# Performance work log

Measured on AMD Instinct MI355X. Metric: run time of the kernel, lower is better.

The kernel has to match this reference:

```python
import jax, jax.numpy as jnp
import numpy as np

B, T, E, H = 4, 2048, 1024, 16
D = E // H
PAD_TOKEN_ID = 0
VOCAB = 50257


def setup_inputs() -> dict:
    key = jax.random.key(0)
    k1, k2, k3, k4 = jax.random.split(key, 4)
    x = jax.random.normal(k1, (B, T, E), dtype=jnp.float32)
    input_ids = jax.random.randint(k2, (B, T), 0, VOCAB, dtype=jnp.int64)
    # guarantee first key of every sequence is non-pad so no softmax row is fully masked
    input_ids = input_ids.at[:, 0].set(1)
    w_qkv = jax.random.normal(k3, (E, 3 * E), dtype=jnp.float32) * 0.02
    w_out = jax.random.normal(k4, (E, E), dtype=jnp.float32) * 0.02
    b_out = jnp.zeros((E,), dtype=jnp.float32)
    return {"x": x, "input_ids": input_ids, "w_qkv": w_qkv, "w_out": w_out, "b_out": b_out}


def reference(x, input_ids, w_qkv, w_out, b_out):
    b, t, e = x.shape
    # fused QKV projection (bias=False in original)
    qkv = x @ w_qkv                                   # [B,T,3E]
    q, k, v = jnp.split(qkv, 3, axis=-1)
    q = q.reshape(b, t, H, D).transpose(0, 2, 1, 3)   # [B,H,T,D]
    k = k.reshape(b, t, H, D).transpose(0, 2, 1, 3)
    v = v.reshape(b, t, H, D).transpose(0, 2, 1, 3)

    scale = 1.0 / jnp.sqrt(jnp.asarray(D, dtype=x.dtype))
    scores = jnp.einsum("bhqd,bhkd->bhqk", q, k) * scale   # [B,H,T,T]

    causal = jnp.tril(jnp.ones((t, t), dtype=bool))         # [T,T]
    key_keep = (input_ids != PAD_TOKEN_ID)[:, None, None, :]  # [B,1,1,T]
    mask = causal[None, None, :, :] & key_keep               # [B,1(T broadcast over H),T,T]
    scores = jnp.where(mask, scores, -jnp.inf)

    attn = jax.nn.softmax(scores, axis=-1)                   # dropout_p=0 in eval
    y = jnp.einsum("bhqk,bhkd->bhqd", attn, v)               # [B,H,T,D]
    y = y.transpose(0, 2, 1, 3).reshape(b, t, e)             # [B,T,E]
    return y @ w_out + b_out
```

## Files before the change

kernel.cpp:

```cpp
#include <hip/hip_runtime.h>
#include <hip/hip_bf16.h>
#include <stdint.h>

#define Hn 16
#define Tn 2048
#define En 1024
#define Dh 64

typedef __bf16 bf16x8 __attribute__((ext_vector_type(8)));
typedef float f32x4 __attribute__((ext_vector_type(4)));
typedef unsigned short u16;
typedef u16 u16x8 __attribute__((ext_vector_type(8)));

#define SCALE_Q 0.18033688f

__device__ __forceinline__ u16 f2bf(float f) {
  __bf16 b = (__bf16)f;
  return __builtin_bit_cast(u16, b);
}

typedef const __attribute__((address_space(1))) void gvoid_t;
typedef __attribute__((address_space(3))) void lvoid_t;
__device__ __forceinline__ void gl_lds16(const void* g, void* l) {
  __builtin_amdgcn_global_load_lds((gvoid_t*)g, (lvoid_t*)l, 16, 0, 0);
}

__global__ void prep_k(const float* __restrict__ x, u16* __restrict__ xb,
                       const int* __restrict__ ids, u16* __restrict__ maskh,
                       const float* __restrict__ wqkv, u16* __restrict__ wqkvt,
                       const float* __restrict__ wout, u16* __restrict__ woutt) {
  __shared__ float tile[32][33];
  __shared__ int is64_s;
  const int blk = blockIdx.x;
  const int tid = threadIdx.x;

  if (blk < 4096) {
    int i = (blk * 256 + tid) * 8;
    float4 a = *(const float4*)(x + i);
    float4 b = *(const float4*)(x + i + 4);
    u16x8 o;
    o[0] = f2bf(a.x); o[1] = f2bf(a.y); o[2] = f2bf(a.z); o[3] = f2bf(a.w);
    o[4] = f2bf(b.x); o[5] = f2bf(b.y); o[6] = f2bf(b.z); o[7] = f2bf(b.w);
    *(u16x8*)(xb + i) = o;
    return;
  }
  if (blk < 4128) {
    if (tid == 0) {
      int all0 = 1;
      for (int i = 1; i < 256; i += 2) all0 &= (ids[i] == 0);
      is64_s = all0;
    }
    __syncthreads();
    int i = (blk - 4096) * 256 + tid;
    int v = is64_s ? ids[2 * i] : ids[i];
    maskh[i] = (v != 0) ? (u16)0 : f2bf(-1e30f);
    return;
  }
  const int t = blk - 4128;
  const int bx = t & 127, by = t >> 7;
  const float* in; u16* out; int C, c0;
  if (bx < 96) { in = wqkv; out = wqkvt; C = 3072; c0 = bx * 32; }
  else         { in = wout; out = woutt; C = 1024; c0 = (bx - 96) * 32; }
  const int r0 = by * 32;
  const int tx = tid & 31, ty = tid >> 5;
  for (int i = ty; i < 32; i += 8)
    tile[i][tx] = in[(size_t)(r0 + i) * C + c0 + tx];
  __syncthreads();
  for (int i = ty; i < 32; i += 8)
    out[(size_t)(c0 + i) * 1024 + r0 + tx] = f2bf(tile[tx][i]);
}

__device__ __forceinline__ void gemm_mainloop(const u16* __restrict__ A,
                                              const u16* __restrict__ Bt,
                                              int K, int m0, int n0,
                                              u16* lds, f32x4 acc[4][4]) {
  const int tid = threadIdx.x;
  const int lane = tid & 63;
  const int w = tid >> 6;
  const int wm = (w >> 1) * 64, wn = (w & 1) * 64;
  const int quad = lane >> 4, ln = lane & 15;

  const int e0 = w * 512 + lane * 8;
  const int r0 = e0 >> 5;
  const int cS = (e0 & 31) ^ (((r0 >> 1) & 3) * 8);

  const u16* gA = A + (size_t)(m0 + r0) * K + cS;
  const u16* gB = Bt + (size_t)(n0 + r0) * K + cS;
  const int xR = ((ln >> 1) & 3) * 8;

  auto stage = [&](int buf, int k0) {
    u16* lA = lds + buf * 8192 + e0;
    u16* lB = lA + 4096;
    gl_lds16(gA + k0, lA);
    gl_lds16(gA + (size_t)64 * K + k0, lA + 2048);
    gl_lds16(gB + k0, lB);
    gl_lds16(gB + (size_t)64 * K + k0, lB + 2048);
  };

  stage(0, 0);
  int cur = 0;
  for (int k0 = 0; k0 < K; k0 += 32) {
    __syncthreads();
    if (k0 + 32 < K) stage(cur ^ 1, k0 + 32);
    const u16* lb = lds + cur * 8192;
    bf16x8 af[4], bfr[4];
#pragma unroll
    for (int mt = 0; mt < 4; mt++)
      af[mt] = *(const bf16x8*)(lb + (wm + mt * 16 + ln) * 32 + ((quad * 8) ^ xR));
#pragma unroll
    for (int nt = 0; nt < 4; nt++)
      bfr[nt] = *(const bf16x8*)(lb + 4096 + (wn + nt * 16 + ln) * 32 + ((quad * 8) ^ xR));
#pragma unroll
    for (int mt = 0; mt < 4; mt++)
#pragma unroll
      for (int nt = 0; nt < 4; nt++)
        acc[mt][nt] = __builtin_amdgcn_mfma_f32_16x16x32_bf16(af[mt], bfr[nt],
                                                              acc[mt][nt], 0, 0, 0);
    cur ^= 1;
  }
  __syncthreads();
}

__global__ __launch_bounds__(256, 4)
void gemm_qkv_kernel(const u16* __restrict__ X, const u16* __restrict__ Wt,
                     u16* __restrict__ Qo, u16* __restrict__ Ko,
                     u16* __restrict__ Vto) {
  __shared__ __align__(16) u16 lds[128 * 130];
  const int m0 = blockIdx.y * 128, n0 = blockIdx.x * 128;
  f32x4 acc[4][4];
#pragma unroll
  for (int i = 0; i < 4; i++)
#pragma unroll
    for (int j = 0; j < 4; j++) acc[i][j] = (f32x4){0.f, 0.f, 0.f, 0.f};

  gemm_mainloop(X, Wt, En, m0, n0, lds, acc);

  const int tid = threadIdx.x, lane = tid & 63, w = tid >> 6;
  const int wm = (w >> 1) * 64, wn = (w & 1) * 64;
  const int quad = lane >> 4, ln = lane & 15;
  const int which = n0 >> 10;
  const int bb = m0 >> 11, t0 = m0 & (Tn - 1);

  if (which < 2) {
#pragma unroll
    for (int mt = 0; mt < 4; mt++)
#pragma unroll
      for (int nt = 0; nt < 4; nt++)
#pragma unroll
        for (int r = 0; r < 4; r++) {
          int t = t0 + wm + mt * 16 + quad * 4 + r;
          int ng = n0 + wn + nt * 16 + ln;
          int e = ng & (En - 1);
          int h = e >> 6, d = e & 63;
          size_t bh = (size_t)(bb * Hn + h);
          if (which == 0)
            Qo[(bh * Tn + t) * Dh + d] = f2bf(acc[mt][nt][r] * SCALE_Q);
          else
            Ko[(bh * Tn + t) * Dh + d] = f2bf(acc[mt][nt][r]);
        }
  } else {
#pragma unroll
    for (int mt = 0; mt < 4; mt++)
#pragma unroll
      for (int nt = 0; nt < 4; nt++)
#pragma unroll
        for (int r = 0; r < 4; r++)
          lds[(wm + mt * 16 + quad * 4 + r) * 130 + wn + nt * 16 + ln] =
              f2bf(acc[mt][nt][r]);
    __syncthreads();
    const int ebase = n0 & (En - 1);
#pragma unroll
    for (int i = 0; i < 32; i++) {
      int col = w * 32 + i;
      int e = ebase + col;
      int hh = e >> 6, d = e & 63;
      size_t vrow = (((size_t)(bb * Hn + hh)) * Dh + d) * Tn + t0;
      Vto[vrow + lane] = lds[lane * 130 + col];
      Vto[vrow + 64 + lane] = lds[(64 + lane) * 130 + col];
    }
  }
}

__global__ __launch_bounds__(256, 4)
void gemm_out_kernel(const u16* __restrict__ Y, const u16* __restrict__ Wt,
                     const float* __restrict__ bias, float* __restrict__ Out) {
  __shared__ __align__(16) u16 lds[16384];
  const int m0 = blockIdx.y * 128, n0 = blockIdx.x * 128;
  f32x4 acc[4][4];
#pragma unroll
  for (int i = 0; i < 4; i++)
#pragma unroll
    for (int j = 0; j < 4; j++) acc[i][j] = (f32x4){0.f, 0.f, 0.f, 0.f};

  gemm_mainloop(Y, Wt, En, m0, n0, lds, acc);

  const int tid = threadIdx.x, lane = tid & 63, w = tid >> 6;
  const int wm = (w >> 1) * 64, wn = (w & 1) * 64;
  const int quad = lane >> 4, ln = lane & 15;

#pragma unroll
  for (int mt = 0; mt < 4; mt++)
#pragma unroll
    for (int nt = 0; nt < 4; nt++)
#pragma unroll
      for (int r = 0; r < 4; r++) {
        int mg = m0 + wm + mt * 16 + quad * 4 + r;
        int ng = n0 + wn + nt * 16 + ln;
        Out[(size_t)mg * En + ng] = acc[mt][nt][r] + bias[ng];
      }
}

__global__ __launch_bounds__(256, 3)
void attn_kernel(const u16* __restrict__ Q, const u16* __restrict__ K,
                 const u16* __restrict__ Vt, const u16* __restrict__ maskh,
                 u16* __restrict__ Y) {
  __shared__ __align__(16) u16 Pl[128 * 76];
  __shared__ __align__(16) u16 KL[2 * 4096];
  __shared__ __align__(16) u16 ML[2048];

  const int bid = blockIdx.x;
  const int g = bid >> 8, sq = (bid >> 6) & 3;
  int qt;
  if (g == 0)      qt = 15 - sq;
  else if (g == 1) qt = sq;
  else if (g == 2) qt = 11 - sq;
  else             qt = 4 + sq;
  const int bh = bid & 63;
  const int b = bh >> 4, h = bh & 15;
  const int tid = threadIdx.x, lane = tid & 63, w = tid >> 6;
  const int quad = lane >> 4, ln = lane & 15;
  const int qb = w * 32;
  const int g0 = qt * 128 + qb;

  const size_t baseQK = (size_t)bh * (Tn * Dh);
  const size_t baseV = (size_t)bh * (Dh * Tn);
  const u16* Kp = K + baseQK;

  const int srow = tid >> 3;
  const int scol = ((tid & 7) * 8) ^ ((srow & 7) * 8);
  const u16* gK0 = Kp + (size_t)srow * Dh + scol;
  const u16* gK1 = Kp + (size_t)(srow + 32) * Dh + scol;
  u16* lK0 = KL + tid * 8;
  u16* lK1 = lK0 + 2048;

  auto stage = [&](int buf, int k0) {
    gl_lds16(gK0 + (size_t)k0 * Dh, lK0 + buf * 4096);
    gl_lds16(gK1 + (size_t)k0 * Dh, lK1 + buf * 4096);
  };

  gl_lds16(maskh + (size_t)b * Tn + tid * 8, ML + tid * 8);

  bf16x8 aq[2][2];
#pragma unroll
  for (int rt = 0; rt < 2; rt++)
#pragma unroll
    for (int ks = 0; ks < 2; ks++)
      aq[rt][ks] = *(const bf16x8*)(Q + baseQK +
          (size_t)(g0 + rt * 16 + ln) * Dh + ks * 32 + quad * 8);

  bf16x8 onesb;
#pragma unroll
  for (int i = 0; i < 8; i++) onesb[i] = (__bf16)1.0f;

  f32x4 O[2][4];
  f32x4 ls[2];
#pragma unroll
  for (int rt = 0; rt < 2; rt++) {
#pragma unroll
    for (int dt = 0; dt < 4; dt++) O[rt][dt] = (f32x4){0.f, 0.f, 0.f, 0.f};
    ls[rt] = (f32x4){0.f, 0.f, 0.f, 0.f};
  }

  auto tile = [&](const u16* kl, int k0, bool dg) {
    f32x4 s[2][4];
    {
      bf16x8 bk[4][2];
      float kvf[4];
#pragma unroll
      for (int ct = 0; ct < 4; ct++) {
        kvf[ct] = __builtin_bit_cast(float,
                      (uint32_t)ML[k0 + ct * 16 + ln] << 16);
#pragma unroll
        for (int ks = 0; ks < 2; ks++)
          bk[ct][ks] = *(const bf16x8*)(kl + (ct * 16 + ln) * 64 +
                                        ((ks * 32 + quad * 8) ^ ((ln & 7) * 8)));
      }
#pragma unroll
      for (int rt = 0; rt < 2; rt++)
#pragma unroll
        for (int ct = 0; ct < 4; ct++)
          s[rt][ct] = (f32x4){kvf[ct], kvf[ct], kvf[ct], kvf[ct]};
      __builtin_amdgcn_s_setprio(1);
#pragma unroll
      for (int ks = 0; ks < 2; ks++)
#pragma unroll
        for (int rt = 0; rt < 2; rt++)
#pragma unroll
          for (int ct = 0; ct < 4; ct++)
            s[rt][ct] = __builtin_amdgcn_mfma_f32_16x16x32_bf16(aq[rt][ks], bk[ct][ks],
                                                                s[rt][ct], 0, 0, 0);
      __builtin_amdgcn_s_setprio(0);
    }

    bf16x8 bv[4][2];
#pragma unroll
    for (int dt = 0; dt < 4; dt++)
#pragma unroll
      for (int ks = 0; ks < 2; ks++)
        bv[dt][ks] = *(const bf16x8*)(Vt + baseV +
            (size_t)(dt * 16 + ln) * Tn + k0 + ks * 32 + quad * 8);

#pragma unroll
    for (int rt = 0; rt < 2; rt++) {
      if (dg) {
#pragma unroll
        for (int ct = 0; ct < 4; ct++)
#pragma unroll
          for (int r = 0; r < 4; r++) {
            int qg = g0 + rt * 16 + quad * 4 + r;
            int kg = k0 + ct * 16 + ln;
            float v = (kg > qg) ? -1e30f : s[rt][ct][r];
            float p = exp2f(v);
            Pl[(qb + rt * 16 + quad * 4 + r) * 76 + ct * 16 + ln] = f2bf(p);
          }
      } else {
#pragma unroll
        for (int ct = 0; ct < 4; ct++)
#pragma unroll
          for (int r = 0; r < 4; r++) {
            float p = exp2f(s[rt][ct][r]);
            Pl[(qb + rt * 16 + quad * 4 + r) * 76 + ct * 16 + ln] = f2bf(p);
          }
      }
    }

    __builtin_amdgcn_s_setprio(1);
#pragma unroll
    for (int ks2 = 0; ks2 < 2; ks2++)
#pragma unroll
      for (int rt = 0; rt < 2; rt++) {
        bf16x8 ap = *(const bf16x8*)(Pl + (qb + rt * 16 + ln) * 76 + ks2 * 32 + quad * 8);
#pragma unroll
        for (int dt = 0; dt < 4; dt++)
          O[rt][dt] = __builtin_amdgcn_mfma_f32_16x16x32_bf16(ap, bv[dt][ks2],
                                                              O[rt][dt], 0, 0, 0);
        ls[rt] = __builtin_amdgcn_mfma_f32_16x16x32_bf16(ap, onesb,
                                                         ls[rt], 0, 0, 0);
      }
    __builtin_amdgcn_s_setprio(0);
  };

  const int nfull = g0 >> 6;
  const int NT = 2 * qt + 1;
  stage(0, 0);
  int cur = 0;
  for (int kt = 0; kt <= NT; kt++) {
    __syncthreads();
    if (kt < NT) stage(cur ^ 1, (kt + 1) * 64);
    if (kt < nfull)       tile(KL + cur * 4096, kt * 64, false);
    else if (kt == nfull) tile(KL + cur * 4096, kt * 64, true);
    cur ^= 1;
  }

#pragma unroll
  for (int rt = 0; rt < 2; rt++)
#pragma unroll
    for (int r = 0; r < 4; r++) {
      float inv = 1.f / ls[rt][r];
      int tg = g0 + rt * 16 + quad * 4 + r;
      size_t ob = ((size_t)b * Tn + tg) * En + h * Dh;
#pragma unroll
      for (int dt = 0; dt < 4; dt++)
        Y[ob + dt * 16 + ln] = f2bf(O[rt][dt][r] * inv);
    }
}

#define OFF_MASK  0
#define OFF_WQKVT 16384
#define OFF_WOUTT (OFF_WQKVT + 3145728)
#define OFF_Q     (OFF_WOUTT + 1048576)
#define OFF_K     (OFF_Q + 8388608)
#define OFF_XY    (OFF_K + 8388608)

extern "C" void kernel_launch(void* const* d_in, const int* in_sizes, int n_in,
                              void* d_out, int out_size, void* d_ws, size_t ws_size,
                              hipStream_t stream) {
  const float* x = nullptr;
  const int* ids_raw = nullptr;
  const float* wqkv = nullptr;
  const float* wout = nullptr;
  const float* bias = nullptr;
  for (int i = 0; i < n_in; i++) {
    switch (in_sizes[i]) {
      case 8388608: x = (const float*)d_in[i]; break;
      case 8192:    ids_raw = (const int*)d_in[i]; break;
      case 3145728: wqkv = (const float*)d_in[i]; break;
      case 1048576: wout = (const float*)d_in[i]; break;
      case 1024:    bias = (const float*)d_in[i]; break;
      default: break;
    }
  }
  if (!x) x = (const float*)d_in[0];
  if (!ids_raw) ids_raw = (const int*)d_in[1];
  if (!wqkv) wqkv = (const float*)d_in[2];
  if (!wout) wout = (const float*)d_in[3];
  if (!bias) bias = (const float*)d_in[4];

  u16* ws = (u16*)d_ws;
  u16* maskh = ws + OFF_MASK;
  u16* wqkv_t = ws + OFF_WQKVT;
  u16* wout_t = ws + OFF_WOUTT;
  u16* Qb = ws + OFF_Q;
  u16* Kb = ws + OFF_K;
  u16* XbYb = ws + OFF_XY;
  u16* Vtb = (u16*)d_out;
  float* out = (float*)d_out;

  prep_k<<<8224, 256, 0, stream>>>(x, XbYb, ids_raw, maskh,
                                   wqkv, wqkv_t, wout, wout_t);
  gemm_qkv_kernel<<<dim3(24, 64), 256, 0, stream>>>(XbYb, wqkv_t, Qb, Kb, Vtb);
  attn_kernel<<<1024, 256, 0, stream>>>(Qb, Kb, Vtb, maskh, XbYb);
  gemm_out_kernel<<<dim3(8, 64), 256, 0, stream>>>(XbYb, wout_t, bias, out);
}
```

Before: 264.1 us.

## Halve attention query tile to 64 rows and launch 2048 blocks longest-first

Each attention block now handles a 64-row query tile, one 16-row slice per wave, instead of 128 rows with two slices per wave. The grid doubles to 2048 blocks, scheduled in descending causal length. The paired triangle scheduling is replaced by a simple longest-first order. This aims at finer load balance and lower register and LDS use for higher occupancy, at the cost of each K/V tile being reused by fewer query rows, so K and V are loaded twice as often per query.

```diff
diff --git a/kernel.cpp b/kernel.cpp
--- a/kernel.cpp
+++ b/kernel.cpp
@@ -214,23 +214,18 @@
 void attn_kernel(const u16* __restrict__ Q, const u16* __restrict__ K,
                  const u16* __restrict__ Vt, const u16* __restrict__ maskh,
                  u16* __restrict__ Y) {
-  __shared__ __align__(16) u16 Pl[128 * 76];
+  __shared__ __align__(16) u16 Pl[64 * 76];
   __shared__ __align__(16) u16 KL[2 * 4096];
   __shared__ __align__(16) u16 ML[2048];
 
   const int bid = blockIdx.x;
-  const int g = bid >> 8, sq = (bid >> 6) & 3;
-  int qt;
-  if (g == 0)      qt = 15 - sq;
-  else if (g == 1) qt = sq;
-  else if (g == 2) qt = 11 - sq;
-  else             qt = 4 + sq;
+  const int qt2 = 31 - (bid >> 6);
   const int bh = bid & 63;
   const int b = bh >> 4, h = bh & 15;
   const int tid = threadIdx.x, lane = tid & 63, w = tid >> 6;
   const int quad = lane >> 4, ln = lane & 15;
-  const int qb = w * 32;
-  const int g0 = qt * 128 + qb;
+  const int qb = w * 16;
+  const int g0 = qt2 * 64 + qb;
 
   const size_t baseQK = (size_t)bh * (Tn * Dh);
   const size_t baseV = (size_t)bh * (Dh * Tn);
@@ -250,29 +245,23 @@
 
   gl_lds16(maskh + (size_t)b * Tn + tid * 8, ML + tid * 8);
 
-  bf16x8 aq[2][2];
-#pragma unroll
-  for (int rt = 0; rt < 2; rt++)
-#pragma unroll
-    for (int ks = 0; ks < 2; ks++)
-      aq[rt][ks] = *(const bf16x8*)(Q + baseQK +
-          (size_t)(g0 + rt * 16 + ln) * Dh + ks * 32 + quad * 8);
+  bf16x8 aq[2];
+#pragma unroll
+  for (int ks = 0; ks < 2; ks++)
+    aq[ks] = *(const bf16x8*)(Q + baseQK +
+        (size_t)(g0 + ln) * Dh + ks * 32 + quad * 8);
 
   bf16x8 onesb;
 #pragma unroll
   for (int i = 0; i < 8; i++) onesb[i] = (__bf16)1.0f;
 
-  f32x4 O[2][4];
-  f32x4 ls[2];
-#pragma unroll
-  for (int rt = 0; rt < 2; rt++) {
-#pragma unroll
-    for (int dt = 0; dt < 4; dt++) O[rt][dt] = (f32x4){0.f, 0.f, 0.f, 0.f};
-    ls[rt] = (f32x4){0.f, 0.f, 0.f, 0.f};
-  }
+  f32x4 O[4];
+  f32x4 ls = (f32x4){0.f, 0.f, 0.f, 0.f};
+#pragma unroll
+  for (int dt = 0; dt < 4; dt++) O[dt] = (f32x4){0.f, 0.f, 0.f, 0.f};
 
   auto tile = [&](const u16* kl, int k0, bool dg) {
-    f32x4 s[2][4];
+    f32x4 s[4];
     {
       bf16x8 bk[4][2];
       float kvf[4];
@@ -286,19 +275,15 @@
                                         ((ks * 32 + quad * 8) ^ ((ln & 7) * 8)));
       }
 #pragma unroll
-      for (int rt = 0; rt < 2; rt++)
+      for (int ct = 0; ct < 4; ct++)
+        s[ct] = (f32x4){kvf[ct], kvf[ct], kvf[ct], kvf[ct]};
+      __builtin_amdgcn_s_setprio(1);
+#pragma unroll
+      for (int ks = 0; ks < 2; ks++)
 #pragma unroll
         for (int ct = 0; ct < 4; ct++)
-          s[rt][ct] = (f32x4){kvf[ct], kvf[ct], kvf[ct], kvf[ct]};
-      __builtin_amdgcn_s_setprio(1);
-#pragma unroll
-      for (int ks = 0; ks < 2; ks++)
-#pragma unroll
-        for (int rt = 0; rt < 2; rt++)
-#pragma unroll
-          for (int ct = 0; ct < 4; ct++)
-            s[rt][ct] = __builtin_amdgcn_mfma_f32_16x16x32_bf16(aq[rt][ks], bk[ct][ks],
-                                                                s[rt][ct], 0, 0, 0);
+          s[ct] = __builtin_amdgcn_mfma_f32_16x16x32_bf16(aq[ks], bk[ct][ks],
+                                                          s[ct], 0, 0, 0);
       __builtin_amdgcn_s_setprio(0);
     }
 
@@ -310,69 +295,59 @@
         bv[dt][ks] = *(const bf16x8*)(Vt + baseV +
             (size_t)(dt * 16 + ln) * Tn + k0 + ks * 32 + quad * 8);
 
-#pragma unroll
-    for (int rt = 0; rt < 2; rt++) {
-      if (dg) {
-#pragma unroll
-        for (int ct = 0; ct < 4; ct++)
-#pragma unroll
-          for (int r = 0; r < 4; r++) {
-            int qg = g0 + rt * 16 + quad * 4 + r;
-            int kg = k0 + ct * 16 + ln;
-            float v = (kg > qg) ? -1e30f : s[rt][ct][r];
-            float p = exp2f(v);
-            Pl[(qb + rt * 16 + quad * 4 + r) * 76 + ct * 16 + ln] = f2bf(p);
-          }
-      } else {
-#pragma unroll
-        for (int ct = 0; ct < 4; ct++)
-#pragma unroll
-          for (int r = 0; r < 4; r++) {
-            float p = exp2f(s[rt][ct][r]);
-            Pl[(qb + rt * 16 + quad * 4 + r) * 76 + ct * 16 + ln] = f2bf(p);
-          }
-      }
+    if (dg) {
+#pragma unroll
+      for (int ct = 0; ct < 4; ct++)
+#pragma unroll
+        for (int r = 0; r < 4; r++) {
+          int qg = g0 + quad * 4 + r;
+          int kg = k0 + ct * 16 + ln;
+          float v = (kg > qg) ? -1e30f : s[ct][r];
+          float p = exp2f(v);
+          Pl[(qb + quad * 4 + r) * 76 + ct * 16 + ln] = f2bf(p);
+        }
+    } else {
+#pragma unroll
+      for (int ct = 0; ct < 4; ct++)
+#pragma unroll
+        for (int r = 0; r < 4; r++) {
+          float p = exp2f(s[ct][r]);
+          Pl[(qb + quad * 4 + r) * 76 + ct * 16 + ln] = f2bf(p);
+        }
     }
 
     __builtin_amdgcn_s_setprio(1);
 #pragma unroll
-    for (int ks2 = 0; ks2 < 2; ks2++)
-#pragma unroll
-      for (int rt = 0; rt < 2; rt++) {
-        bf16x8 ap = *(const bf16x8*)(Pl + (qb + rt * 16 + ln) * 76 + ks2 * 32 + quad * 8);
-#pragma unroll
-        for (int dt = 0; dt < 4; dt++)
-          O[rt][dt] = __builtin_amdgcn_mfma_f32_16x16x32_bf16(ap, bv[dt][ks2],
-                                                              O[rt][dt], 0, 0, 0);
-        ls[rt] = __builtin_amdgcn_mfma_f32_16x16x32_bf16(ap, onesb,
-                                                         ls[rt], 0, 0, 0);
-      }
+    for (int ks2 = 0; ks2 < 2; ks2++) {
+      bf16x8 ap = *(const bf16x8*)(Pl + (qb + ln) * 76 + ks2 * 32 + quad * 8);
+#pragma unroll
+      for (int dt = 0; dt < 4; dt++)
+        O[dt] = __builtin_amdgcn_mfma_f32_16x16x32_bf16(ap, bv[dt][ks2],
+                                                        O[dt], 0, 0, 0);
+      ls = __builtin_amdgcn_mfma_f32_16x16x32_bf16(ap, onesb, ls, 0, 0, 0);
+    }
     __builtin_amdgcn_s_setprio(0);
   };
 
-  const int nfull = g0 >> 6;
-  const int NT = 2 * qt + 1;
   stage(0, 0);
   int cur = 0;
-  for (int kt = 0; kt <= NT; kt++) {
+  for (int kt = 0; kt <= qt2; kt++) {
     __syncthreads();
-    if (kt < NT) stage(cur ^ 1, (kt + 1) * 64);
-    if (kt < nfull)       tile(KL + cur * 4096, kt * 64, false);
-    else if (kt == nfull) tile(KL + cur * 4096, kt * 64, true);
+    if (kt < qt2) stage(cur ^ 1, (kt + 1) * 64);
+    if (kt < qt2) tile(KL + cur * 4096, kt * 64, false);
+    else          tile(KL + cur * 4096, kt * 64, true);
     cur ^= 1;
   }
 
 #pragma unroll
-  for (int rt = 0; rt < 2; rt++)
-#pragma unroll
-    for (int r = 0; r < 4; r++) {
-      float inv = 1.f / ls[rt][r];
-      int tg = g0 + rt * 16 + quad * 4 + r;
-      size_t ob = ((size_t)b * Tn + tg) * En + h * Dh;
-#pragma unroll
-      for (int dt = 0; dt < 4; dt++)
-        Y[ob + dt * 16 + ln] = f2bf(O[rt][dt][r] * inv);
-    }
+  for (int r = 0; r < 4; r++) {
+    float inv = 1.f / ls[r];
+    int tg = g0 + quad * 4 + r;
+    size_t ob = ((size_t)b * Tn + tg) * En + h * Dh;
+#pragma unroll
+    for (int dt = 0; dt < 4; dt++)
+      Y[ob + dt * 16 + ln] = f2bf(O[dt][r] * inv);
+  }
 }
 
 #define OFF_MASK  0
@@ -419,6 +394,6 @@
   prep_k<<<8224, 256, 0, stream>>>(x, XbYb, ids_raw, maskh,
                                    wqkv, wqkv_t, wout, wout_t);
   gemm_qkv_kernel<<<dim3(24, 64), 256, 0, stream>>>(XbYb, wqkv_t, Qb, Kb, Vtb);
-  attn_kernel<<<1024, 256, 0, stream>>>(Qb, Kb, Vtb, maskh, XbYb);
+  attn_kernel<<<2048, 256, 0, stream>>>(Qb, Kb, Vtb, maskh, XbYb);
   gemm_out_kernel<<<dim3(8, 64), 256, 0, stream>>>(XbYb, wout_t, bias, out);
 }
```

Result: slower. 327.3 us (+23.9%).
